# Kernel optimization log

Measured on AMD Instinct MI355X. Metric: run time of the kernel, lower is better.

Reference implementation:

```python
import jax, jax.numpy as jnp
import numpy as np
from jax.ops import segment_sum

N_NODES = 10000
N_EDGES = 160000
HIDDEN = 128
NUM_RBF = 32
NUM_LAYERS = 2
LATENT = 64
N_GRAPHS = 128
CUTOFF = 5.0
EPS = 1e-8


def expnorm_rbf(r):
    # ExpNormalSmearing (ViSNet default RBF) with cosine cutoff
    means = jnp.linspace(jnp.exp(-CUTOFF), 1.0, NUM_RBF)          # [R]
    beta = (2.0 / NUM_RBF * (1.0 - jnp.exp(-CUTOFF))) ** -2
    cut = 0.5 * (jnp.cos(jnp.pi * r / CUTOFF) + 1.0) * (r < CUTOFF)
    return cut[:, None] * jnp.exp(-beta * (jnp.exp(-r)[:, None] - means) ** 2)  # [E,R]


def setup_inputs() -> dict:
    key = jax.random.key(0)
    ks = jax.random.split(key, 16)
    z = jax.random.randint(ks[0], (N_NODES,), 0, 100)
    pos = jax.random.normal(ks[1], (N_NODES, 3), jnp.float32) * 2.0
    batch = jnp.sort(jax.random.randint(ks[2], (N_NODES,), 0, N_GRAPHS))
    edge_index = jax.random.randint(ks[3], (2, N_EDGES), 0, N_NODES)
    H, R, L = HIDDEN, NUM_RBF, NUM_LAYERS
    s = lambda fan: 1.0 / np.sqrt(fan)
    embed_table = jax.random.normal(ks[4], (100, H), jnp.float32)
    W_rbf = jax.random.normal(ks[5], (L, R, H), jnp.float32) * s(R)
    W1 = jax.random.normal(ks[6], (L, H, H), jnp.float32) * s(H)
    Wo = jax.random.normal(ks[7], (L, H, H), jnp.float32) * s(H)
    Wv = jax.random.normal(ks[8], (L, H, H), jnp.float32) * s(H)
    Wvec1 = jax.random.normal(ks[9], (H, H), jnp.float32) * s(H)
    Wvec2 = jax.random.normal(ks[10], (H, H), jnp.float32) * s(H)
    W_a = jax.random.normal(ks[11], (2 * H, H), jnp.float32) * s(2 * H)
    b_a = jnp.zeros((H,), jnp.float32)
    W_b = jax.random.normal(ks[12], (H, LATENT + 1), jnp.float32) * s(H)
    b_b = jnp.zeros((LATENT + 1,), jnp.float32)
    # MSE-stability init fix from the torch module:
    # scalar_linear.bias[-1] = -1.0 ; scalar_linear.weight[-1] *= 0.1
    b_b = b_b.at[-1].set(-1.0)
    W_b = W_b.at[:, -1].multiply(0.1)
    return dict(z=z, pos=pos, batch=batch, edge_index=edge_index,
                embed_table=embed_table, W_rbf=W_rbf, W1=W1, Wo=Wo, Wv=Wv,
                Wvec1=Wvec1, Wvec2=Wvec2, W_a=W_a, b_a=b_a, W_b=W_b, b_b=b_b)


def reference(z, pos, batch, edge_index, embed_table, W_rbf, W1, Wo, Wv,
              Wvec1, Wvec2, W_a, b_a, W_b, b_b):
    src, dst = edge_index[0], edge_index[1]
    # edge geometry (computed once, shared across layers)
    d = pos[dst] - pos[src]                      # [E,3]
    r = jnp.sqrt(jnp.sum(d * d, axis=-1) + EPS)  # [E]
    dirn = d / r[:, None]                        # [E,3]
    rbf = expnorm_rbf(r)                         # [E,R]

    x = embed_table[z]                           # [N,H] scalar features
    vec = jnp.zeros((x.shape[0], 3, HIDDEN), x.dtype)  # [N,3,H] equivariant features

    for l in range(NUM_LAYERS):
        filt = rbf @ W_rbf[l]                                        # [E,H] radial filter
        phi = jax.nn.silu((x[src] * filt) @ W1[l])                   # [E,H] edge message
        dx = segment_sum(phi, dst, num_segments=N_NODES)             # scatter-add
        x = x + dx @ Wo[l]
        vmix = jnp.einsum('nch,hk->nck', vec, Wv[l])                 # [N,3,H]
        vmsg = vmix[src] * filt[:, None, :] + phi[:, None, :] * dirn[:, :, None]  # [E,3,H]
        vec = vec + segment_sum(vmsg, dst, num_segments=N_NODES)

    # gated-equivariant output head (pre_reduce -> [N, latent+1] scalars)
    v2 = jnp.einsum('nch,hk->nck', vec, Wvec2)
    vnorm = jnp.sqrt(jnp.sum(v2 * v2, axis=1) + EPS)                 # [N,H]
    a = jax.nn.silu(jnp.concatenate([x, vnorm], axis=-1) @ W_a + b_a)
    out = a @ W_b + b_b                                              # [N, latent+1]

    pooled = segment_sum(out, batch, num_segments=N_GRAPHS)          # global_add_pool
    mu = pooled[:, :LATENT]
    log_var = jnp.clip(pooled[:, LATENT:LATENT + 1], -10.0, 2.0)
    return mu, log_var
```

## Files before the change

### kernel.cpp

```cpp
#include <hip/hip_runtime.h>
#include <math.h>

#define N_NODES 10000
#define N_EDGES 160000
#define HIDDEN 128
#define NUM_RBF 32
#define LATENT 64
#define N_GRAPHS 128
#define CUTOFF 5.0f
#define EPS 1e-8f

#define NBLK_N 157

typedef __attribute__((ext_vector_type(8))) short short8;
typedef __attribute__((ext_vector_type(4))) float f32x4;
typedef unsigned short ushort_t;

__device__ __forceinline__ float fast_silu(float v) {
    return v * __builtin_amdgcn_rcpf(1.0f + __expf(-v));
}

__device__ __forceinline__ ushort_t f2bf(float f) {
    union { float f; unsigned u; } v;
    v.f = f;
    unsigned r = v.u + 0x7FFFu + ((v.u >> 16) & 1u);
    return (ushort_t)(r >> 16);
}
__device__ __forceinline__ float bf2f(ushort_t u) {
    union { unsigned u; float f; } v;
    v.u = ((unsigned)u) << 16;
    return v.f;
}

__global__ void init_kernel(const int* __restrict__ z, const float* __restrict__ embed,
                            float* __restrict__ x, ushort_t* __restrict__ x16,
                            float* __restrict__ vec, float* __restrict__ dxb,
                            float* __restrict__ pooled, int* __restrict__ deg,
                            const float* __restrict__ W1, const float* __restrict__ Wrbf,
                            const float* __restrict__ Wv, const float* __restrict__ Wo,
                            const float* __restrict__ Wvec2, const float* __restrict__ W_a,
                            const float* __restrict__ W_b, ushort_t* __restrict__ W1T,
                            ushort_t* __restrict__ WrbfT, ushort_t* __restrict__ WvT,
                            ushort_t* __restrict__ WoT, ushort_t* __restrict__ Wvec2T,
                            ushort_t* __restrict__ W_aT, ushort_t* __restrict__ W_bT) {
    if (blockIdx.x < 15000) {
        int i = blockIdx.x * 256 + threadIdx.x;
        if (i < N_NODES * 384) vec[i] = 0.0f;
        if (i < N_NODES * 128) {
            float v = embed[z[i >> 7] * 128 + (i & 127)];
            x[i] = v;
            x16[i] = f2bf(v);
            dxb[i] = 0.0f;
        }
        if (i < N_NODES) deg[i] = 0;
        if (i < N_GRAPHS * (LATENT + 1)) pooled[i] = 0.0f;
        return;
    }
    int i = (blockIdx.x - 15000) * 256 + threadIdx.x;
    if (i < 2 * 128 * 128) {
        int l = i >> 14;
        int n = (i & 16383) >> 7;
        int k = i & 127;
        W1T[i] = f2bf(W1[l * 16384 + k * 128 + n]);
        WvT[i] = f2bf(Wv[l * 16384 + k * 128 + n]);
        WoT[i] = f2bf(Wo[l * 16384 + k * 128 + n]);
    }
    if (i < 2 * 128 * 32) {
        int l = i >> 12;
        int n = (i & 4095) >> 5;
        int k = i & 31;
        WrbfT[i] = f2bf(Wrbf[l * 4096 + k * 128 + n]);
    }
    if (i < 128 * 128) {
        int n = i >> 7;
        int k = i & 127;
        Wvec2T[i] = f2bf(Wvec2[k * 128 + n]);
    }
    if (i < 128 * 256) {
        int n = i >> 8;
        int k = i & 255;
        W_aT[i] = f2bf(W_a[k * 128 + n]);
    }
    if (i < 80 * 128) {
        int n = i >> 7;
        int k = i & 127;
        W_bT[i] = (n < LATENT + 1) ? f2bf(W_b[k * (LATENT + 1) + n]) : (ushort_t)0;
    }
}

__global__ void hist_kernel(const int* __restrict__ dst, int* __restrict__ deg) {
    int e = blockIdx.x * blockDim.x + threadIdx.x;
    if (e < N_EDGES) atomicAdd(&deg[dst[e]], 1);
}

__global__ void prefix_kernel(const int* __restrict__ deg, int* __restrict__ cursor) {
    __shared__ int part[1024];
    const int ITEMS = 10;
    int t = threadIdx.x;
    int base = t * ITEMS;
    int local[ITEMS];
    int s = 0;
#pragma unroll
    for (int j = 0; j < ITEMS; j++) {
        int idx = base + j;
        int v = (idx < N_NODES) ? deg[idx] : 0;
        local[j] = s;
        s += v;
    }
    part[t] = s;
    __syncthreads();
    for (int off = 1; off < 1024; off <<= 1) {
        int v = (t >= off) ? part[t - off] : 0;
        __syncthreads();
        part[t] += v;
        __syncthreads();
    }
    int base_sum = (t > 0) ? part[t - 1] : 0;
#pragma unroll
    for (int j = 0; j < ITEMS; j++) {
        int idx = base + j;
        if (idx < N_NODES) cursor[idx] = base_sum + local[j];
    }
}

__global__ void scatter_geom_kernel(const int* __restrict__ ei, const float* __restrict__ pos,
                                    int* __restrict__ cursor, int* __restrict__ sperm,
                                    int* __restrict__ dperm, ushort_t* __restrict__ rbf16,
                                    float* __restrict__ dirn) {
    int e = blockIdx.x * blockDim.x + threadIdx.x;
    if (e >= N_EDGES) return;
    int s = ei[e];
    int t = ei[N_EDGES + e];
    int p = atomicAdd(&cursor[t], 1);
    sperm[p] = s;
    dperm[p] = t;

    float dx = pos[t * 3 + 0] - pos[s * 3 + 0];
    float dy = pos[t * 3 + 1] - pos[s * 3 + 1];
    float dz = pos[t * 3 + 2] - pos[s * 3 + 2];
    float r = sqrtf(dx * dx + dy * dy + dz * dz + EPS);
    float inv = 1.0f / r;
    dirn[p * 3 + 0] = dx * inv;
    dirn[p * 3 + 1] = dy * inv;
    dirn[p * 3 + 2] = dz * inv;

    float e5 = __expf(-CUTOFF);
    float span = 1.0f - e5;
    float b = (2.0f / NUM_RBF) * span;
    float beta = 1.0f / (b * b);
    float cut = (r < CUTOFF) ? 0.5f * (__cosf((float)M_PI * r / CUTOFF) + 1.0f) : 0.0f;
    float er = __expf(-r);
#pragma unroll
    for (int k = 0; k < NUM_RBF; k++) {
        float mean = e5 + span * ((float)k / (NUM_RBF - 1));
        float d = er - mean;
        rbf16[(size_t)p * 32 + k] = f2bf(cut * __expf(-beta * d * d));
    }
}

template <int K, int EPI>
__device__ __forceinline__ void gemm_body(ushort_t* As, float* __restrict__ A,
                                          const ushort_t* __restrict__ WT,
                                          const float* __restrict__ bias,
                                          const float* __restrict__ Cin, float* __restrict__ C,
                                          ushort_t* __restrict__ C16, int M, int bx, int tid) {
    constexpr int STR = K + 8;
    int row0 = bx * 64;
    int w = tid >> 6;
    int lane = tid & 63;
    int c = lane & 15;
    int q = lane >> 4;
    int wr0 = w * 16;

    {
        int r = wr0 + (lane >> 2);
        int row = row0 + r;
        int segbase = (lane & 3) * (K / 4);
#pragma unroll
        for (int u = 0; u < K / 16; u++) {
            int k0 = segbase + u * 4;
            float4 v = make_float4(0.f, 0.f, 0.f, 0.f);
            if (row < M) v = *(const float4*)(A + (size_t)row * 128 + k0);
            ushort_t b4[4] = {f2bf(v.x), f2bf(v.y), f2bf(v.z), f2bf(v.w)};
            *(uint2*)(As + r * STR + k0) = *(uint2*)b4;
        }
        if ((EPI & 16) && row < M) {
            float4 z4 = make_float4(0.f, 0.f, 0.f, 0.f);
#pragma unroll
            for (int u = 0; u < 8; u++)
                *(float4*)(A + (size_t)row * 128 + (lane & 3) * 32 + u * 4) = z4;
        }
    }

    f32x4 acc[8] = {};
#pragma unroll
    for (int s = 0; s < K / 32; s++) {
        short8 af = *(const short8*)(As + (wr0 + c) * STR + s * 32 + q * 8);
#pragma unroll
        for (int t8 = 0; t8 < 8; t8++) {
            short8 bf = *(const short8*)(WT + (size_t)(t8 * 16 + c) * K + s * 32 + q * 8);
            acc[t8] = __builtin_amdgcn_mfma_f32_16x16x32_bf16(af, bf, acc[t8], 0, 0, 0);
        }
    }

    if (EPI & 8) {
#pragma unroll
        for (int t8 = 0; t8 < 8; t8++) {
#pragma unroll
            for (int r4 = 0; r4 < 4; r4++) {
                int lrow = wr0 + q * 4 + r4;
                As[lrow * STR + t8 * 16 + c] = f2bf(acc[t8][r4]);
            }
        }
#pragma unroll
        for (int i = 0; i < 4; i++) {
            int slot = lane + i * 64;
            int rl = slot >> 4;
            int c8 = slot & 15;
            int row = row0 + wr0 + rl;
            if (row < M)
                *(uint4*)((ushort_t*)C + (size_t)row * 128 + c8 * 8) =
                    *(uint4*)(As + (wr0 + rl) * STR + c8 * 8);
        }
    } else {
#pragma unroll
        for (int t8 = 0; t8 < 8; t8++) {
#pragma unroll
            for (int r4 = 0; r4 < 4; r4++) {
                int row = row0 + wr0 + q * 4 + r4;
                if (row < M) {
                    int col = t8 * 16 + c;
                    float o = acc[t8][r4];
                    if (EPI & 1) o += bias[col];
                    if (EPI & 2) o += Cin[(size_t)row * 128 + col];
                    if (EPI & 4) o = fast_silu(o);
                    C[(size_t)row * 128 + col] = o;
                    if (EPI & 64) C16[(size_t)row * 128 + col] = f2bf(o);
                }
            }
        }
    }
}

__global__ __launch_bounds__(256, 4) void combo1_kernel(float* __restrict__ dxb,
                                                        const ushort_t* __restrict__ WoT0,
                                                        float* __restrict__ x,
                                                        ushort_t* __restrict__ x16,
                                                        float* __restrict__ vec,
                                                        const ushort_t* __restrict__ WvT1,
                                                        ushort_t* __restrict__ vmix16) {
    __shared__ ushort_t As[64 * 136];
    if (blockIdx.x < NBLK_N)
        gemm_body<128, 2 | 16 | 64>(As, dxb, WoT0, nullptr, x, x, x16, N_NODES, blockIdx.x,
                                    threadIdx.x);
    else
        gemm_body<128, 8>(As, vec, WvT1, nullptr, nullptr, (float*)vmix16, nullptr, N_NODES * 3,
                          blockIdx.x - NBLK_N, threadIdx.x);
}

__global__ __launch_bounds__(256, 4) void combo2_kernel(float* __restrict__ dxb,
                                                        const ushort_t* __restrict__ WoT1,
                                                        float* __restrict__ x,
                                                        float* __restrict__ vec,
                                                        const ushort_t* __restrict__ Wvec2T,
                                                        float* __restrict__ vbuf) {
    __shared__ ushort_t As[64 * 136];
    if (blockIdx.x < NBLK_N)
        gemm_body<128, 2>(As, dxb, WoT1, nullptr, x, x, nullptr, N_NODES, blockIdx.x,
                          threadIdx.x);
    else
        gemm_body<128, 0>(As, vec, Wvec2T, nullptr, nullptr, vbuf, nullptr, N_NODES * 3,
                          blockIdx.x - NBLK_N, threadIdx.x);
}

__global__ __launch_bounds__(256, 4) void wa_pool_kernel(const float* __restrict__ x,
                                                         const float* __restrict__ vbuf,
                                                         const ushort_t* __restrict__ W_aT,
                                                         const float* __restrict__ b_a,
                                                         const ushort_t* __restrict__ W_bT,
                                                         const float* __restrict__ b_b,
                                                         const int* __restrict__ batch,
                                                         float* __restrict__ pooled, int M) {
    __shared__ ushort_t As[64 * 264];
    __shared__ int s_b[64];
    int tid = threadIdx.x;
    int row0 = blockIdx.x * 64;
    int w = tid >> 6;
    int lane = tid & 63;
    int c = lane & 15;
    int q = lane >> 4;
    int wr0 = w * 16;

    if (lane < 16) {
        int row = row0 + wr0 + lane;
        s_b[wr0 + lane] = (row < M) ? batch[row] : 0;
    }
    {
        int r = wr0 + (lane >> 2);
        int row = row0 + r;
        int segbase = (lane & 3) * 64;
#pragma unroll
        for (int u = 0; u < 16; u++) {
            int k0 = segbase + u * 4;
            float4 v = make_float4(0.f, 0.f, 0.f, 0.f);
            if (row < M) {
                if (k0 >= 128) {
                    const float* vb = vbuf + (size_t)row * 384 + (k0 - 128);
                    float4 va = *(const float4*)(vb);
                    float4 vb2 = *(const float4*)(vb + 128);
                    float4 vc = *(const float4*)(vb + 256);
                    v.x = sqrtf(va.x * va.x + vb2.x * vb2.x + vc.x * vc.x + EPS);
                    v.y = sqrtf(va.y * va.y + vb2.y * vb2.y + vc.y * vc.y + EPS);
                    v.z = sqrtf(va.z * va.z + vb2.z * vb2.z + vc.z * vc.z + EPS);
                    v.w = sqrtf(va.w * va.w + vb2.w * vb2.w + vc.w * vc.w + EPS);
                } else {
                    v = *(const float4*)(x + (size_t)row * 128 + k0);
                }
            }
            ushort_t b4[4] = {f2bf(v.x), f2bf(v.y), f2bf(v.z), f2bf(v.w)};
            *(uint2*)(As + r * 264 + k0) = *(uint2*)b4;
        }
    }

    f32x4 acc[8] = {};
#pragma unroll
    for (int s = 0; s < 8; s++) {
        short8 af = *(const short8*)(As + (wr0 + c) * 264 + s * 32 + q * 8);
#pragma unroll
        for (int t8 = 0; t8 < 8; t8++) {
            short8 bf = *(const short8*)(W_aT + (size_t)(t8 * 16 + c) * 256 + s * 32 + q * 8);
            acc[t8] = __builtin_amdgcn_mfma_f32_16x16x32_bf16(af, bf, acc[t8], 0, 0, 0);
        }
    }

#pragma unroll
    for (int t8 = 0; t8 < 8; t8++) {
#pragma unroll
        for (int r4 = 0; r4 < 4; r4++) {
            int col = t8 * 16 + c;
            float o = fast_silu(acc[t8][r4] + b_a[col]);
            As[(wr0 + q * 4 + r4) * 264 + col] = f2bf(o);
        }
    }

    f32x4 acc2[5] = {};
#pragma unroll
    for (int s = 0; s < 4; s++) {
        short8 af = *(const short8*)(As + (wr0 + c) * 264 + s * 32 + q * 8);
#pragma unroll
        for (int t5 = 0; t5 < 5; t5++) {
            short8 bf = *(const short8*)(W_bT + (size_t)(t5 * 16 + c) * 128 + s * 32 + q * 8);
            acc2[t5] = __builtin_amdgcn_mfma_f32_16x16x32_bf16(af, bf, acc2[t5], 0, 0, 0);
        }
    }
#pragma unroll
    for (int t5 = 0; t5 < 5; t5++) {
        int col = t5 * 16 + c;
        if (col < LATENT + 1) {
            float bb = b_b[col];
#pragma unroll
            for (int r4 = 0; r4 < 4; r4++) {
                int rl = wr0 + q * 4 + r4;
                if (row0 + rl < M)
                    atomicAdd(&pooled[s_b[rl] * (LATENT + 1) + col], acc2[t5][r4] + bb);
            }
        }
    }
}

template <bool HASV>
__global__ __launch_bounds__(256, 4) void edge_fused(
    const ushort_t* __restrict__ rbf16, const ushort_t* __restrict__ WrbfT,
    const ushort_t* __restrict__ x16, const int* __restrict__ sperm,
    const int* __restrict__ dperm, const ushort_t* __restrict__ W1T,
    const float* __restrict__ dirn, const ushort_t* __restrict__ vmix,
    float* __restrict__ dxb, float* __restrict__ vec) {
    __shared__ __align__(16) char smem_raw[36864];
    ushort_t* Ts = (ushort_t*)smem_raw;
    ushort_t* PhiT = (ushort_t*)smem_raw;
    ushort_t* FiltT = (ushort_t*)(smem_raw + 18432);
    __shared__ int s_src[64];
    __shared__ int s_dst[64];
    __shared__ __align__(16) float s_dir4[256];

    int tid = threadIdx.x;
    int row0 = blockIdx.x * 64;
    int w = tid >> 6;
    int lane = tid & 63;
    int c = lane & 15;
    int q = lane >> 4;
    int wr0 = w * 16;

    if (lane < 16) {
        s_src[wr0 + lane] = sperm[row0 + wr0 + lane];
        s_dst[wr0 + lane] = dperm[row0 + wr0 + lane];
    }
    if (w == 3) {
        const float* dp = dirn + (size_t)(row0 + lane) * 3;
        s_dir4[lane * 4 + 0] = dp[0];
        s_dir4[lane * 4 + 1] = dp[1];
        s_dir4[lane * 4 + 2] = dp[2];
        s_dir4[lane * 4 + 3] = 0.f;
    }

    int srow[4];
#pragma unroll
    for (int r = 0; r < 4; r++) srow[r] = sperm[row0 + wr0 + q * 4 + r];
    ushort_t xv[4][8];
#pragma unroll
    for (int r = 0; r < 4; r++) {
        const ushort_t* xp = x16 + (size_t)srow[r] * 128 + c;
#pragma unroll
        for (int t8 = 0; t8 < 8; t8++) xv[r][t8] = xp[t8 * 16];
    }

    f32x4 facc[8];
    {
        short8 af = *(const short8*)(rbf16 + (size_t)(row0 + wr0 + c) * 32 + q * 8);
#pragma unroll
        for (int t8 = 0; t8 < 8; t8++) {
            short8 bfr = *(const short8*)(WrbfT + (size_t)(t8 * 16 + c) * 32 + q * 8);
            f32x4 z = {};
            facc[t8] = __builtin_amdgcn_mfma_f32_16x16x32_bf16(af, bfr, z, 0, 0, 0);
        }
    }

#pragma unroll
    for (int t8 = 0; t8 < 8; t8++) {
#pragma unroll
        for (int r = 0; r < 4; r++) {
            int row = wr0 + q * 4 + r;
            Ts[row * 136 + t8 * 16 + c] = f2bf(facc[t8][r] * bf2f(xv[r][t8]));
        }
    }

    f32x4 pacc[8] = {};
    const ushort_t* ap = Ts + (wr0 + c) * 136 + q * 8;
#pragma unroll
    for (int s = 0; s < 4; s++) {
        short8 af = *(const short8*)(ap + s * 32);
#pragma unroll
        for (int t8 = 0; t8 < 8; t8++) {
            short8 bfr = *(const short8*)(W1T + (size_t)(t8 * 16 + c) * 128 + s * 32 + q * 8);
            pacc[t8] = __builtin_amdgcn_mfma_f32_16x16x32_bf16(af, bfr, pacc[t8], 0, 0, 0);
        }
    }
    __syncthreads();

#pragma unroll
    for (int t8 = 0; t8 < 8; t8++) {
        int col = t8 * 16 + c;
        ushort_t pb[4];
#pragma unroll
        for (int r = 0; r < 4; r++) pb[r] = f2bf(fast_silu(pacc[t8][r]));
        *(uint2*)(PhiT + col * 72 + wr0 + q * 4) = *(uint2*)pb;
        if (HASV) {
            ushort_t fb[4];
#pragma unroll
            for (int r = 0; r < 4; r++) fb[r] = f2bf(facc[t8][r]);
            *(uint2*)(FiltT + col * 72 + wr0 + q * 4) = *(uint2*)fb;
        }
    }
    __syncthreads();

    int h = tid & 127;
    int half = tid >> 7;
    int rbeg = half * 32;
    float adx = 0.f, a0 = 0.f, a1 = 0.f, a2 = 0.f;
    int cur = s_dst[rbeg];
#pragma unroll
    for (int g = 0; g < 4; g++) {
        ushort_t ph[8], fl[8];
        *(uint4*)ph = *(const uint4*)(PhiT + h * 72 + rbeg + g * 8);
        if (HASV) *(uint4*)fl = *(const uint4*)(FiltT + h * 72 + rbeg + g * 8);
        float v0[8], v1[8], v2[8];
        if (HASV) {
#pragma unroll
            for (int j = 0; j < 8; j++) {
                const ushort_t* vm = vmix + (size_t)s_src[rbeg + g * 8 + j] * 384 + h;
                v0[j] = bf2f(vm[0]);
                v1[j] = bf2f(vm[128]);
                v2[j] = bf2f(vm[256]);
            }
        }
#pragma unroll
        for (int j = 0; j < 8; j++) {
            int r = rbeg + g * 8 + j;
            int d = s_dst[r];
            if (d != cur) {
                atomicAdd(&dxb[(size_t)cur * 128 + h], adx);
                atomicAdd(&vec[((size_t)cur * 3 + 0) * 128 + h], a0);
                atomicAdd(&vec[((size_t)cur * 3 + 1) * 128 + h], a1);
                atomicAdd(&vec[((size_t)cur * 3 + 2) * 128 + h], a2);
                cur = d;
                adx = a0 = a1 = a2 = 0.f;
            }
            float p = bf2f(ph[j]);
            float4 dd = *(const float4*)(s_dir4 + r * 4);
            adx += p;
            if (HASV) {
                float f = bf2f(fl[j]);
                a0 += v0[j] * f + p * dd.x;
                a1 += v1[j] * f + p * dd.y;
                a2 += v2[j] * f + p * dd.z;
            } else {
                a0 += p * dd.x;
                a1 += p * dd.y;
                a2 += p * dd.z;
            }
        }
    }
    atomicAdd(&dxb[(size_t)cur * 128 + h], adx);
    atomicAdd(&vec[((size_t)cur * 3 + 0) * 128 + h], a0);
    atomicAdd(&vec[((size_t)cur * 3 + 1) * 128 + h], a1);
    atomicAdd(&vec[((size_t)cur * 3 + 2) * 128 + h], a2);
}

__global__ void finalize_kernel(const float* __restrict__ pooled, float* __restrict__ out) {
    int i = blockIdx.x * blockDim.x + threadIdx.x;
    if (i >= N_GRAPHS * (LATENT + 1)) return;
    int g = i / (LATENT + 1);
    int k = i % (LATENT + 1);
    float v = pooled[i];
    if (k < LATENT) {
        out[g * LATENT + k] = v;
    } else {
        v = fminf(fmaxf(v, -10.0f), 2.0f);
        out[N_GRAPHS * LATENT + g] = v;
    }
}

extern "C" void kernel_launch(void* const* d_in, const int* in_sizes, int n_in,
                              void* d_out, int out_size, void* d_ws, size_t ws_size,
                              hipStream_t stream) {
    const int* z = (const int*)d_in[0];
    const float* pos = (const float*)d_in[1];
    const int* batch = (const int*)d_in[2];
    const int* ei = (const int*)d_in[3];
    const float* embed = (const float*)d_in[4];
    const float* W_rbf = (const float*)d_in[5];
    const float* W1 = (const float*)d_in[6];
    const float* Wo = (const float*)d_in[7];
    const float* Wv = (const float*)d_in[8];
    const float* Wvec2 = (const float*)d_in[10];
    const float* W_a = (const float*)d_in[11];
    const float* b_a = (const float*)d_in[12];
    const float* W_b = (const float*)d_in[13];
    const float* b_b = (const float*)d_in[14];
    float* out = (float*)d_out;

    const int* dsts = ei + N_EDGES;

    float* ws = (float*)d_ws;
    float* dirn = ws;
    float* x = dirn + (size_t)N_EDGES * 3;
    float* vec = x + (size_t)N_NODES * 128;
    float* vbuf = vec + (size_t)N_NODES * 384;
    float* dxb = vbuf + (size_t)N_NODES * 384;
    float* pooled = dxb + (size_t)N_NODES * 128;
    ushort_t* x16 = (ushort_t*)(pooled + N_GRAPHS * (LATENT + 1) + 16);
    ushort_t* rbf16 = x16 + (size_t)N_NODES * 128;
    ushort_t* vmix16 = rbf16 + (size_t)N_EDGES * 32;
    ushort_t* W1T = vmix16 + (size_t)N_NODES * 384;
    ushort_t* WrbfT = W1T + 2 * 16384;
    ushort_t* WvT = WrbfT + 2 * 4096;
    ushort_t* WoT = WvT + 2 * 16384;
    ushort_t* Wvec2T = WoT + 2 * 16384;
    ushort_t* W_aT = Wvec2T + 16384;
    ushort_t* W_bT = W_aT + 32768;
    int* ibase = (int*)(W_bT + 80 * 128);
    int* deg = ibase;
    int* cursor = deg + N_NODES;
    int* sperm = cursor + N_NODES;
    int* dperm = sperm + N_EDGES;

    init_kernel<<<15000 + 128, 256, 0, stream>>>(z, embed, x, x16, vec, dxb, pooled, deg, W1,
                                                 W_rbf, Wv, Wo, Wvec2, W_a, W_b, W1T, WrbfT, WvT,
                                                 WoT, Wvec2T, W_aT, W_bT);
    hist_kernel<<<(N_EDGES + 255) / 256, 256, 0, stream>>>(dsts, deg);
    prefix_kernel<<<1, 1024, 0, stream>>>(deg, cursor);
    scatter_geom_kernel<<<(N_EDGES + 255) / 256, 256, 0, stream>>>(ei, pos, cursor, sperm, dperm,
                                                                   rbf16, dirn);

    edge_fused<false><<<N_EDGES / 64, 256, 0, stream>>>(rbf16, WrbfT, x16, sperm, dperm, W1T,
                                                        dirn, nullptr, dxb, vec);
    combo1_kernel<<<NBLK_N + (N_NODES * 3 + 63) / 64, 256, 0, stream>>>(dxb, WoT, x, x16, vec,
                                                                        WvT + 16384, vmix16);
    edge_fused<true><<<N_EDGES / 64, 256, 0, stream>>>(rbf16, WrbfT + 4096, x16, sperm, dperm,
                                                       W1T + 16384, dirn, vmix16, dxb, vec);
    combo2_kernel<<<NBLK_N + (N_NODES * 3 + 63) / 64, 256, 0, stream>>>(dxb, WoT + 16384, x, vec,
                                                                        Wvec2T, vbuf);
    wa_pool_kernel<<<NBLK_N, 256, 0, stream>>>(x, vbuf, W_aT, b_a, W_bT, b_b, batch, pooled,
                                               N_NODES);
    finalize_kernel<<<(N_GRAPHS * (LATENT + 1) + 255) / 256, 256, 0, stream>>>(pooled, out);
}
```

Measured before the change: 339.1 us.

## Split output head over more blocks and prefetch vmix gathers in edge kernel

The gated output head now runs on 16-row blocks (625 blocks instead of 157), with the four waves splitting the W_a column tiles and then the W_b tiles. This spreads a small, latency-bound GEMM over more of the GPU. In the edge scatter loop, the vmix gathers for the next 8-edge group are double-buffered in registers so they are issued ahead of use, and destination indices are loaded as vectors from shared memory. The no-vector edge variant also declares half as much shared memory, which may allow more blocks per CU, at the cost of higher register pressure from the prefetch buffers.

```diff
diff --git a/kernel.cpp b/kernel.cpp
--- a/kernel.cpp
+++ b/kernel.cpp
@@ -273,16 +273,105 @@
                           blockIdx.x - NBLK_N, threadIdx.x);
 }
 
-__global__ __launch_bounds__(256, 4) void wa_pool_kernel(const float* __restrict__ x,
-                                                         const float* __restrict__ vbuf,
-                                                         const ushort_t* __restrict__ W_aT,
-                                                         const float* __restrict__ b_a,
-                                                         const ushort_t* __restrict__ W_bT,
-                                                         const float* __restrict__ b_b,
-                                                         const int* __restrict__ batch,
-                                                         float* __restrict__ pooled, int M) {
-    __shared__ ushort_t As[64 * 264];
-    __shared__ int s_b[64];
+__global__ __launch_bounds__(256) void wa_pool_kernel(const float* __restrict__ x,
+                                                      const float* __restrict__ vbuf,
+                                                      const ushort_t* __restrict__ W_aT,
+                                                      const float* __restrict__ b_a,
+                                                      const ushort_t* __restrict__ W_bT,
+                                                      const float* __restrict__ b_b,
+                                                      const int* __restrict__ batch,
+                                                      float* __restrict__ pooled) {
+    __shared__ ushort_t As[16 * 264];
+    __shared__ ushort_t A2[16 * 136];
+    __shared__ int s_b[16];
+    int tid = threadIdx.x;
+    int row0 = blockIdx.x * 16;
+    int w = tid >> 6;
+    int lane = tid & 63;
+    int c = lane & 15;
+    int q = lane >> 4;
+
+    if (tid < 16) s_b[tid] = batch[row0 + tid];
+    {
+        int r = tid >> 4;
+        int seg = (tid & 15) * 16;
+        int row = row0 + r;
+#pragma unroll
+        for (int u = 0; u < 4; u++) {
+            int k0 = seg + u * 4;
+            float4 v;
+            if (k0 >= 128) {
+                const float* vb = vbuf + (size_t)row * 384 + (k0 - 128);
+                float4 va = *(const float4*)(vb);
+                float4 vb2 = *(const float4*)(vb + 128);
+                float4 vc = *(const float4*)(vb + 256);
+                v.x = sqrtf(va.x * va.x + vb2.x * vb2.x + vc.x * vc.x + EPS);
+                v.y = sqrtf(va.y * va.y + vb2.y * vb2.y + vc.y * vc.y + EPS);
+                v.z = sqrtf(va.z * va.z + vb2.z * vb2.z + vc.z * vc.z + EPS);
+                v.w = sqrtf(va.w * va.w + vb2.w * vb2.w + vc.w * vc.w + EPS);
+            } else {
+                v = *(const float4*)(x + (size_t)row * 128 + k0);
+            }
+            ushort_t b4[4] = {f2bf(v.x), f2bf(v.y), f2bf(v.z), f2bf(v.w)};
+            *(uint2*)(As + r * 264 + k0) = *(uint2*)b4;
+        }
+    }
+    __syncthreads();
+
+    f32x4 acc[2] = {};
+#pragma unroll
+    for (int s = 0; s < 8; s++) {
+        short8 af = *(const short8*)(As + c * 264 + s * 32 + q * 8);
+#pragma unroll
+        for (int i = 0; i < 2; i++) {
+            int t8 = 2 * w + i;
+            short8 bf = *(const short8*)(W_aT + (size_t)(t8 * 16 + c) * 256 + s * 32 + q * 8);
+            acc[i] = __builtin_amdgcn_mfma_f32_16x16x32_bf16(af, bf, acc[i], 0, 0, 0);
+        }
+    }
+#pragma unroll
+    for (int i = 0; i < 2; i++) {
+#pragma unroll
+        for (int r4 = 0; r4 < 4; r4++) {
+            int col = (2 * w + i) * 16 + c;
+            A2[(q * 4 + r4) * 136 + col] = f2bf(fast_silu(acc[i][r4] + b_a[col]));
+        }
+    }
+    __syncthreads();
+
+    for (int t5 = w; t5 < 5; t5 += 4) {
+        f32x4 acc2 = {};
+#pragma unroll
+        for (int s = 0; s < 4; s++) {
+            short8 af = *(const short8*)(A2 + c * 136 + s * 32 + q * 8);
+            short8 bf = *(const short8*)(W_bT + (size_t)(t5 * 16 + c) * 128 + s * 32 + q * 8);
+            acc2 = __builtin_amdgcn_mfma_f32_16x16x32_bf16(af, bf, acc2, 0, 0, 0);
+        }
+        int col = t5 * 16 + c;
+        if (col < LATENT + 1) {
+            float bb = b_b[col];
+#pragma unroll
+            for (int r4 = 0; r4 < 4; r4++)
+                atomicAdd(&pooled[s_b[q * 4 + r4] * (LATENT + 1) + col], acc2[r4] + bb);
+        }
+    }
+}
+
+template <bool HASV>
+__global__ __launch_bounds__(256, 4) void edge_fused(
+    const ushort_t* __restrict__ rbf16, const ushort_t* __restrict__ WrbfT,
+    const ushort_t* __restrict__ x16, const int* __restrict__ sperm,
+    const int* __restrict__ dperm, const ushort_t* __restrict__ W1T,
+    const float* __restrict__ dirn, const ushort_t* __restrict__ vmix,
+    float* __restrict__ dxb, float* __restrict__ vec) {
+    __shared__ __align__(16) char smem_raw[HASV ? 36864 : 18432];
+    ushort_t* Ts = (ushort_t*)smem_raw;
+    ushort_t* PhiT = (ushort_t*)smem_raw;
+    ushort_t* FiltT = (ushort_t*)(smem_raw + 18432);
+    __shared__ __align__(16) int s_src[64];
+    __shared__ __align__(16) int s_dst[64];
+    __shared__ __align__(16) float s_dir4[256];
+
     int tid = threadIdx.x;
     int row0 = blockIdx.x * 64;
     int w = tid >> 6;
@@ -292,106 +381,6 @@
     int wr0 = w * 16;
 
     if (lane < 16) {
-        int row = row0 + wr0 + lane;
-        s_b[wr0 + lane] = (row < M) ? batch[row] : 0;
-    }
-    {
-        int r = wr0 + (lane >> 2);
-        int row = row0 + r;
-        int segbase = (lane & 3) * 64;
-#pragma unroll
-        for (int u = 0; u < 16; u++) {
-            int k0 = segbase + u * 4;
-            float4 v = make_float4(0.f, 0.f, 0.f, 0.f);
-            if (row < M) {
-                if (k0 >= 128) {
-                    const float* vb = vbuf + (size_t)row * 384 + (k0 - 128);
-                    float4 va = *(const float4*)(vb);
-                    float4 vb2 = *(const float4*)(vb + 128);
-                    float4 vc = *(const float4*)(vb + 256);
-                    v.x = sqrtf(va.x * va.x + vb2.x * vb2.x + vc.x * vc.x + EPS);
-                    v.y = sqrtf(va.y * va.y + vb2.y * vb2.y + vc.y * vc.y + EPS);
-                    v.z = sqrtf(va.z * va.z + vb2.z * vb2.z + vc.z * vc.z + EPS);
-                    v.w = sqrtf(va.w * va.w + vb2.w * vb2.w + vc.w * vc.w + EPS);
-                } else {
-                    v = *(const float4*)(x + (size_t)row * 128 + k0);
-                }
-            }
-            ushort_t b4[4] = {f2bf(v.x), f2bf(v.y), f2bf(v.z), f2bf(v.w)};
-            *(uint2*)(As + r * 264 + k0) = *(uint2*)b4;
-        }
-    }
-
-    f32x4 acc[8] = {};
-#pragma unroll
-    for (int s = 0; s < 8; s++) {
-        short8 af = *(const short8*)(As + (wr0 + c) * 264 + s * 32 + q * 8);
-#pragma unroll
-        for (int t8 = 0; t8 < 8; t8++) {
-            short8 bf = *(const short8*)(W_aT + (size_t)(t8 * 16 + c) * 256 + s * 32 + q * 8);
-            acc[t8] = __builtin_amdgcn_mfma_f32_16x16x32_bf16(af, bf, acc[t8], 0, 0, 0);
-        }
-    }
-
-#pragma unroll
-    for (int t8 = 0; t8 < 8; t8++) {
-#pragma unroll
-        for (int r4 = 0; r4 < 4; r4++) {
-            int col = t8 * 16 + c;
-            float o = fast_silu(acc[t8][r4] + b_a[col]);
-            As[(wr0 + q * 4 + r4) * 264 + col] = f2bf(o);
-        }
-    }
-
-    f32x4 acc2[5] = {};
-#pragma unroll
-    for (int s = 0; s < 4; s++) {
-        short8 af = *(const short8*)(As + (wr0 + c) * 264 + s * 32 + q * 8);
-#pragma unroll
-        for (int t5 = 0; t5 < 5; t5++) {
-            short8 bf = *(const short8*)(W_bT + (size_t)(t5 * 16 + c) * 128 + s * 32 + q * 8);
-            acc2[t5] = __builtin_amdgcn_mfma_f32_16x16x32_bf16(af, bf, acc2[t5], 0, 0, 0);
-        }
-    }
-#pragma unroll
-    for (int t5 = 0; t5 < 5; t5++) {
-        int col = t5 * 16 + c;
-        if (col < LATENT + 1) {
-            float bb = b_b[col];
-#pragma unroll
-            for (int r4 = 0; r4 < 4; r4++) {
-                int rl = wr0 + q * 4 + r4;
-                if (row0 + rl < M)
-                    atomicAdd(&pooled[s_b[rl] * (LATENT + 1) + col], acc2[t5][r4] + bb);
-            }
-        }
-    }
-}
-
-template <bool HASV>
-__global__ __launch_bounds__(256, 4) void edge_fused(
-    const ushort_t* __restrict__ rbf16, const ushort_t* __restrict__ WrbfT,
-    const ushort_t* __restrict__ x16, const int* __restrict__ sperm,
-    const int* __restrict__ dperm, const ushort_t* __restrict__ W1T,
-    const float* __restrict__ dirn, const ushort_t* __restrict__ vmix,
-    float* __restrict__ dxb, float* __restrict__ vec) {
-    __shared__ __align__(16) char smem_raw[36864];
-    ushort_t* Ts = (ushort_t*)smem_raw;
-    ushort_t* PhiT = (ushort_t*)smem_raw;
-    ushort_t* FiltT = (ushort_t*)(smem_raw + 18432);
-    __shared__ int s_src[64];
-    __shared__ int s_dst[64];
-    __shared__ __align__(16) float s_dir4[256];
-
-    int tid = threadIdx.x;
-    int row0 = blockIdx.x * 64;
-    int w = tid >> 6;
-    int lane = tid & 63;
-    int c = lane & 15;
-    int q = lane >> 4;
-    int wr0 = w * 16;
-
-    if (lane < 16) {
         s_src[wr0 + lane] = sperm[row0 + wr0 + lane];
         s_dst[wr0 + lane] = dperm[row0 + wr0 + lane];
     }
@@ -467,26 +456,46 @@
     int half = tid >> 7;
     int rbeg = half * 32;
     float adx = 0.f, a0 = 0.f, a1 = 0.f, a2 = 0.f;
+
+    float v0[2][8], v1[2][8], v2[2][8];
+    if (HASV) {
+        int sg[8];
+        *(uint4*)&sg[0] = *(const uint4*)&s_src[rbeg];
+        *(uint4*)&sg[4] = *(const uint4*)&s_src[rbeg + 4];
+#pragma unroll
+        for (int j = 0; j < 8; j++) {
+            const ushort_t* vm = vmix + (size_t)sg[j] * 384 + h;
+            v0[0][j] = bf2f(vm[0]);
+            v1[0][j] = bf2f(vm[128]);
+            v2[0][j] = bf2f(vm[256]);
+        }
+    }
     int cur = s_dst[rbeg];
 #pragma unroll
     for (int g = 0; g < 4; g++) {
+        int cb = g & 1, nb = cb ^ 1;
+        if (HASV && g < 3) {
+            int sg[8];
+            *(uint4*)&sg[0] = *(const uint4*)&s_src[rbeg + (g + 1) * 8];
+            *(uint4*)&sg[4] = *(const uint4*)&s_src[rbeg + (g + 1) * 8 + 4];
+#pragma unroll
+            for (int j = 0; j < 8; j++) {
+                const ushort_t* vm = vmix + (size_t)sg[j] * 384 + h;
+                v0[nb][j] = bf2f(vm[0]);
+                v1[nb][j] = bf2f(vm[128]);
+                v2[nb][j] = bf2f(vm[256]);
+            }
+        }
+        int da[8];
+        *(uint4*)&da[0] = *(const uint4*)&s_dst[rbeg + g * 8];
+        *(uint4*)&da[4] = *(const uint4*)&s_dst[rbeg + g * 8 + 4];
         ushort_t ph[8], fl[8];
         *(uint4*)ph = *(const uint4*)(PhiT + h * 72 + rbeg + g * 8);
         if (HASV) *(uint4*)fl = *(const uint4*)(FiltT + h * 72 + rbeg + g * 8);
-        float v0[8], v1[8], v2[8];
-        if (HASV) {
-#pragma unroll
-            for (int j = 0; j < 8; j++) {
-                const ushort_t* vm = vmix + (size_t)s_src[rbeg + g * 8 + j] * 384 + h;
-                v0[j] = bf2f(vm[0]);
-                v1[j] = bf2f(vm[128]);
-                v2[j] = bf2f(vm[256]);
-            }
-        }
 #pragma unroll
         for (int j = 0; j < 8; j++) {
             int r = rbeg + g * 8 + j;
-            int d = s_dst[r];
+            int d = da[j];
             if (d != cur) {
                 atomicAdd(&dxb[(size_t)cur * 128 + h], adx);
                 atomicAdd(&vec[((size_t)cur * 3 + 0) * 128 + h], a0);
@@ -500,9 +509,9 @@
             adx += p;
             if (HASV) {
                 float f = bf2f(fl[j]);
-                a0 += v0[j] * f + p * dd.x;
-                a1 += v1[j] * f + p * dd.y;
-                a2 += v2[j] * f + p * dd.z;
+                a0 += v0[cb][j] * f + p * dd.x;
+                a1 += v1[cb][j] * f + p * dd.y;
+                a2 += v2[cb][j] * f + p * dd.z;
             } else {
                 a0 += p * dd.x;
                 a1 += p * dd.y;
@@ -590,7 +599,7 @@
                                                        W1T + 16384, dirn, vmix16, dxb, vec);
     combo2_kernel<<<NBLK_N + (N_NODES * 3 + 63) / 64, 256, 0, stream>>>(dxb, WoT + 16384, x, vec,
                                                                         Wvec2T, vbuf);
-    wa_pool_kernel<<<NBLK_N, 256, 0, stream>>>(x, vbuf, W_aT, b_a, W_bT, b_b, batch, pooled,
-                                               N_NODES);
+    wa_pool_kernel<<<N_NODES / 16, 256, 0, stream>>>(x, vbuf, W_aT, b_a, W_bT, b_b, batch,
+                                                     pooled);
     finalize_kernel<<<(N_GRAPHS * (LATENT + 1) + 255) / 256, 256, 0, stream>>>(pooled, out);
 }
```

New measurement: 323.5 us. 1.05x faster.
